# Kernel tuning notes

Measured on AMD Instinct MI355X. Metric: run time of the kernel, lower is better.

Reference implementation:

```python
import jax, jax.numpy as jnp
import numpy as np

N_NODES = 50000
N_EDGES = 800000
NUM_GRAPHS = 256
H = 128          # h_dim
C = H + 1        # CGConv channels = 129
Z = 2 * C + 1    # concat(x_i, x_j, edge_attr) = 259
N_GRAPH_LAYERS = 5
N_FC = 3
OUT_DIM = 1


def setup_inputs() -> dict:
    key = jax.random.key(0)
    ks = jax.random.split(key, 12)
    atoms = jax.random.randint(ks[0], (N_NODES,), 0, 119)
    pos = jax.random.normal(ks[1], (N_NODES, 3), dtype=jnp.float32)
    edge_index = jax.random.randint(ks[2], (2, N_EDGES), 0, N_NODES)
    batch = jnp.sort(jax.random.randint(ks[3], (N_NODES,), 0, NUM_GRAPHS))
    s = 0.05
    emb = jax.random.normal(ks[4], (119, H), dtype=jnp.float32)
    Wf = jax.random.normal(ks[5], (N_GRAPH_LAYERS, Z, C), dtype=jnp.float32) * s
    bf = jnp.zeros((N_GRAPH_LAYERS, C), dtype=jnp.float32)
    Ws = jax.random.normal(ks[6], (N_GRAPH_LAYERS, Z, C), dtype=jnp.float32) * s
    bs = jnp.zeros((N_GRAPH_LAYERS, C), dtype=jnp.float32)
    Wfc = jax.random.normal(ks[7], (N_FC, C, C), dtype=jnp.float32) * s
    bfc = jnp.zeros((N_FC, C), dtype=jnp.float32)
    Wout = jax.random.normal(ks[8], (C, OUT_DIM), dtype=jnp.float32) * s
    bout = jnp.zeros((OUT_DIM,), dtype=jnp.float32)
    return {"atoms": atoms, "pos": pos, "edge_index": edge_index, "batch": batch,
            "emb": emb, "Wf": Wf, "bf": bf, "Ws": Ws, "bs": bs,
            "Wfc": Wfc, "bfc": bfc, "Wout": Wout, "bout": bout}


def reference(atoms, pos, edge_index, batch, emb, Wf, bf, Ws, bs, Wfc, bfc, Wout, bout):
    n = atoms.shape[0]
    src, dst = edge_index[0], edge_index[1]  # PyG: x_j = x[src], x_i = x[dst], aggregate at dst
    # edge_attr = ||pos[src] - pos[dst]||, shape [E, 1]
    edge_attr = jnp.linalg.norm(pos[src] - pos[dst], axis=-1, keepdims=True)
    # node features: atom embedding + z-coordinate -> [N, 129]
    x = jnp.concatenate([emb[atoms], pos[:, 2:3]], axis=-1)
    for l in range(Wf.shape[0]):
        z = jnp.concatenate([x[dst], x[src], edge_attr], axis=-1)  # [E, 259]
        m = jax.nn.sigmoid(z @ Wf[l] + bf[l]) * jax.nn.softplus(z @ Ws[l] + bs[l])
        x = x + jax.ops.segment_sum(m, dst, num_segments=n)  # CGConv: aggr='add' + residual
    # mean pooling per graph
    sums = jax.ops.segment_sum(x, batch, num_segments=NUM_GRAPHS)
    cnts = jax.ops.segment_sum(jnp.ones((n, 1), x.dtype), batch, num_segments=NUM_GRAPHS)
    g = sums / jnp.maximum(cnts, 1.0)
    for l in range(Wfc.shape[0]):
        g = g @ Wfc[l] + bfc[l]
    return g @ Wout + bout
```

## Files before the change

kernel.cpp:

```cpp
#include <hip/hip_runtime.h>
#include <math.h>

#define N_NODES 50000
#define N_EDGES 800000
#define NUM_GRAPHS 256
#define NPADROWS 50048
#define CAP 64
#define SCLN -1.44269504088896f
#define SCLP 1.44269504088896f
#define C693 0.69314718056f
#define LROW 264

typedef __attribute__((ext_vector_type(8))) short short8;
typedef __attribute__((ext_vector_type(4))) float f32x4;
typedef __attribute__((ext_vector_type(2))) float f32x2;

__device__ __forceinline__ float fast_rcp(float x) {
#if __has_builtin(__builtin_amdgcn_rcpf)
  return __builtin_amdgcn_rcpf(x);
#else
  return 1.0f / x;
#endif
}
__device__ __forceinline__ float EX2(float x) {
#if __has_builtin(__builtin_amdgcn_exp2f)
  return __builtin_amdgcn_exp2f(x);
#else
  return exp2f(x);
#endif
}
__device__ __forceinline__ float LG2(float x) {
#if __has_builtin(__builtin_amdgcn_logf)
  return __builtin_amdgcn_logf(x);
#else
  return log2f(x);
#endif
}
__device__ __forceinline__ unsigned f2bf(float x) {
  unsigned u = __float_as_uint(x);
  return (u + 0x7fffu + ((u >> 16) & 1u)) >> 16;
}
__device__ __forceinline__ unsigned short bfr(float v) {
  return (unsigned short)((__float_as_uint(v) + 0x8000u) >> 16);
}
__device__ __forceinline__ unsigned pkbfr(float lo, float hi) {
  unsigned a = (__float_as_uint(lo) + 0x8000u) >> 16;
  unsigned b = (__float_as_uint(hi) + 0x8000u) & 0xffff0000u;
  return a | b;
}
__device__ __forceinline__ float u2f(unsigned u) { return __uint_as_float(u); }
__device__ __forceinline__ f32x2 mk2(float a, float b) {
  f32x2 r; r.x = a; r.y = b; return r;
}
__device__ __forceinline__ f32x2 unp(unsigned u) {
  return mk2(u2f(u << 16), u2f(u & 0xffff0000u));
}
__device__ __forceinline__ void edge_ch2(f32x2 gf, f32x2 gs, float cmul, f32x2& acc) {
  f32x2 den = mk2(EX2(gf.x), EX2(gf.y)) + 1.0f;
  f32x2 lg = mk2(LG2(1.0f + EX2(-fabsf(gs.x))), LG2(1.0f + EX2(-fabsf(gs.y))));
  f32x2 sp = lg + __builtin_elementwise_max(gs, (f32x2)0.0f);
  f32x2 rt = mk2(fast_rcp(den.x), fast_rcp(den.y)) * sp;
  acc = __builtin_elementwise_fma(rt, (f32x2)cmul, acc);
}

__global__ void init_x(const int* __restrict__ atoms, const float* __restrict__ pos,
                       const float* __restrict__ emb, float* __restrict__ x128c,
                       unsigned* __restrict__ xbu, float4* __restrict__ pos4,
                       int* __restrict__ cnt) {
  int n = blockIdx.x;
  int t = threadIdx.x;
  int a = atoms[n];
  float2 e = *(const float2*)(emb + (size_t)a * 128 + 2 * t);
  xbu[(size_t)n * 64 + t] = f2bf(e.x) | (f2bf(e.y) << 16);
  if (t == 0) x128c[n] = pos[n * 3 + 2];
  if (t == 1) pos4[n] = make_float4(pos[3 * n], pos[3 * n + 1], pos[3 * n + 2], 0.f);
  if (t == 2) cnt[n] = 0;
}

__global__ void prep_b(const float* __restrict__ Wf, const float* __restrict__ Ws,
                       const float* __restrict__ bfp, const float* __restrict__ bsp,
                       uint4* __restrict__ Bp, float2* __restrict__ Wtail) {
  int idx = blockIdx.x * 256 + threadIdx.x;
  if (idx < 5 * 4 * 9 * 4 * 64) {
    int lane = idx & 63;
    int t = idx >> 6;
    int ks = t & 3; t >>= 2;
    int ct = t % 9; t /= 9;
    int g = t & 3;
    int l = t >> 2;
    const float* W = (g >= 2) ? Ws : Wf;
    float sc = (g < 2) ? SCLN : SCLP;
    int col = ct * 16 + (lane & 15);
    int kb = ks * 32 + (lane >> 4) * 8;
    unsigned u[4];
#pragma unroll
    for (int p = 0; p < 4; ++p) {
      unsigned lo = 0, hi = 0;
      if (col < 129) {
        int k0 = kb + 2 * p, k1 = k0 + 1;
        int r0 = (g & 1) ? 129 + k0 : k0;
        int r1 = (g & 1) ? 129 + k1 : k1;
        lo = f2bf(sc * W[(size_t)(l * 259 + r0) * 129 + col]);
        hi = f2bf(sc * W[(size_t)(l * 259 + r1) * 129 + col]);
      }
      u[p] = lo | (hi << 16);
    }
    Bp[idx] = make_uint4(u[0], u[1], u[2], u[3]);
  } else {
    int j = idx - 5 * 4 * 9 * 4 * 64;
    if (j >= 5 * 4 * 144) return;
    int c = j % 144;
    int t = j / 144;
    int g = t & 3;
    int l = t >> 2;
    float sc = (g < 2) ? SCLN : SCLP;
    float w1 = 0.0f, bias = 0.0f;
    if (c <= 128) {
      const float* W = (g >= 2) ? Ws : Wf;
      int row = (g & 1) ? 257 : 128;
      w1 = sc * W[(size_t)(l * 259 + row) * 129 + c];
      if (g == 0) bias = SCLN * bfp[l * 129 + c];
      if (g == 2) bias = SCLP * bsp[l * 129 + c];
    }
    Wtail[(l * 4 + g) * 144 + c] = make_float2(w1, bias);
  }
}

__global__ void build_csr(const int* __restrict__ ei, const float4* __restrict__ pos4,
                          const int* __restrict__ batch, int* __restrict__ cnt,
                          int2* __restrict__ csr, int* __restrict__ goff) {
  int e = blockIdx.x * 256 + threadIdx.x;
  if (e <= N_NODES) {
    int b = (e < N_NODES) ? batch[e] : NUM_GRAPHS;
    int bp = (e > 0) ? batch[e - 1] : -1;
    for (int g = bp + 1; g <= b; ++g) goff[g] = e;
  }
  if (e >= N_EDGES) return;
  int s = ei[e];
  int d = ei[N_EDGES + e];
  float4 ps = pos4[s];
  float4 pd = pos4[d];
  float dx = ps.x - pd.x, dy = ps.y - pd.y, dz = ps.z - pd.z;
  float ea = sqrtf(dx * dx + dy * dy + dz * dz);
  int p = atomicAdd(&cnt[d], 1);
  if (p < CAP) csr[d * CAP + p] = make_int2(s, __float_as_int(ea));
}

__global__ __launch_bounds__(256) void gemm_mfma(
    const unsigned* __restrict__ xbu, const float* __restrict__ x128c,
    const uint4* __restrict__ Bp, const float2* __restrict__ Wtail,
    unsigned short* __restrict__ Pdh, unsigned short* __restrict__ Pfs,
    unsigned* __restrict__ Pd128c, unsigned* __restrict__ Pc128, int layer) {
  __shared__ short smA[32 * 136];
  __shared__ unsigned short ldsD[32 * LROW];
  __shared__ unsigned short ldsS[32 * LROW];
  int n0 = blockIdx.x * 32;
  int tid = threadIdx.x;
  for (int ch = tid; ch < 512; ch += 256) {
    int row = ch >> 4, cq = ch & 15;
    *(uint4*)(&smA[row * 136 + cq * 8]) =
        *(const uint4*)(xbu + (size_t)(n0 + row) * 64 + cq * 4);
  }
  __syncthreads();
  int g = tid >> 6;
  int l = tid & 63;
  int q = l >> 4, c16 = l & 15;
  const short8* Bp8 = (const short8*)Bp;
  int bbase = (layer * 4 + g) * 9 * 4;
  f32x4 acc[2][9];
#pragma unroll
  for (int rt = 0; rt < 2; ++rt)
#pragma unroll
    for (int ct = 0; ct < 9; ++ct) acc[rt][ct] = (f32x4){0.f, 0.f, 0.f, 0.f};
#pragma unroll
  for (int ks = 0; ks < 4; ++ks) {
    short8 a0 = *(const short8*)(&smA[c16 * 136 + (ks * 4 + q) * 8]);
    short8 a1 = *(const short8*)(&smA[(16 + c16) * 136 + (ks * 4 + q) * 8]);
#pragma unroll
    for (int ct = 0; ct < 9; ++ct) {
      short8 b = Bp8[(size_t)(bbase + ct * 4 + ks) * 64 + l];
      acc[0][ct] = __builtin_amdgcn_mfma_f32_16x16x32_bf16(a0, b, acc[0][ct], 0, 0, 0);
      acc[1][ct] = __builtin_amdgcn_mfma_f32_16x16x32_bf16(a1, b, acc[1][ct], 0, 0, 0);
    }
  }
  const float2* Wt = Wtail + (layer * 4 + g) * 144;
  float x128[2][4];
#pragma unroll
  for (int rt = 0; rt < 2; ++rt)
#pragma unroll
    for (int r = 0; r < 4; ++r)
      x128[rt][r] = x128c[n0 + rt * 16 + q * 4 + r];
  unsigned short* ldsO = (g & 1) ? ldsS : ldsD;
  int soff = (g >= 2) ? 2 : 0;
  unsigned short* c128p = (g & 1) ? (unsigned short*)Pc128 : (unsigned short*)Pd128c;
  int c128o = (g >= 2) ? 1 : 0;
#pragma unroll
  for (int ct = 0; ct < 9; ++ct) {
    int col = ct * 16 + c16;
    float2 wb = Wt[col];
#pragma unroll
    for (int rt = 0; rt < 2; ++rt) {
#pragma unroll
      for (int r = 0; r < 4; ++r) {
        int rl = rt * 16 + q * 4 + r;
        float v = acc[rt][ct][r] + fmaf(x128[rt][r], wb.x, wb.y);
        if (col < 128) {
          ldsO[rl * LROW + ((col >> 1) << 2) + soff + (col & 1)] = bfr(v);
        } else if (col == 128) {
          c128p[2 * (size_t)(n0 + rl) + c128o] = bfr(v);
        }
      }
    }
  }
  __syncthreads();
#pragma unroll
  for (int i = tid; i < 2048; i += 256) {
    int img = i >> 10;
    int c = i & 1023;
    int row = c >> 5, part = c & 31;
    const unsigned short* src = (img ? ldsS : ldsD) + row * LROW + part * 8;
    unsigned short* dst = (img ? Pfs : Pdh) + (size_t)(n0 + row) * 256 + part * 8;
    *(uint4*)dst = *(const uint4*)src;
  }
}

__global__ __launch_bounds__(256) void edge_agg(
    const unsigned short* __restrict__ Pdh, const unsigned short* __restrict__ Pfs,
    const unsigned* __restrict__ Pd128c, const unsigned* __restrict__ Pc128,
    unsigned* __restrict__ xbu, float* __restrict__ x128c, const int* __restrict__ cnt,
    const int2* __restrict__ csr, const float* __restrict__ WfL,
    const float* __restrict__ WsL) {
  int lane = threadIdx.x & 63;
  int half = lane >> 5;
  int l5 = lane & 31;
  int n = blockIdx.x * 4 + (threadIdx.x >> 6);
  if (n >= N_NODES) return;
  int nu = __builtin_amdgcn_readfirstlane(n);
  const float* wfl = WfL + 258 * 129;
  const float* wsl = WsL + 258 * 129;
  uint4 pdv = *(const uint4*)(Pdh + (size_t)nu * 256 + 8 * l5);
  f32x2 bfa = unp(pdv.x), bsa = unp(pdv.y), bfb = unp(pdv.z), bsb = unp(pdv.w);
  float2 wfa0 = *(const float2*)(wfl + 4 * l5);
  float2 wfb0 = *(const float2*)(wfl + 4 * l5 + 2);
  float2 wsa0 = *(const float2*)(wsl + 4 * l5);
  float2 wsb0 = *(const float2*)(wsl + 4 * l5 + 2);
  f32x2 wfa = mk2(SCLN * wfa0.x, SCLN * wfa0.y), wfb = mk2(SCLN * wfb0.x, SCLN * wfb0.y);
  f32x2 wsa = mk2(SCLP * wsa0.x, SCLP * wsa0.y), wsb = mk2(SCLP * wsb0.x, SCLP * wsb0.y);
  unsigned pd1 = Pd128c[nu];
  float bfc8 = u2f(pd1 << 16), bsc8 = u2f(pd1 & 0xffff0000u);
  float wfc8 = SCLN * wfl[128], wsc8 = SCLP * wsl[128];
  int m = cnt[nu];
  if (m > CAP) m = CAP;
  const int4* cb4 = (const int4*)(csr + (size_t)nu * CAP);
  const uint4* Pfq = (const uint4*)Pfs;
  float maskC = half ? 0.0f : C693;
  f32x2 accA = (f32x2)0.0f, accB = (f32x2)0.0f;

#define GATHER(qq) Pfq[(size_t)(half ? qq.z : qq.x) * 32 + l5]
#define COMPUTE(qq, gg, CM)                                                    \
  {                                                                            \
    f32x2 ea_ = (f32x2)__int_as_float(half ? qq.w : qq.y);                     \
    edge_ch2(__builtin_elementwise_fma(ea_, wfa, bfa + unp(gg.x)),             \
             __builtin_elementwise_fma(ea_, wsa, bsa + unp(gg.y)), CM, accA);  \
    edge_ch2(__builtin_elementwise_fma(ea_, wfb, bfb + unp(gg.z)),             \
             __builtin_elementwise_fma(ea_, wsb, bsb + unp(gg.w)), CM, accB);  \
  }

  int Pf = m >> 1;
  int4 qc = make_int4(0, 0, 0, 0);
  uint4 gc = make_uint4(0, 0, 0, 0);
  if (Pf > 0) {
    qc = cb4[0];
    gc = GATHER(qc);
  }
  for (int p = 0; p < Pf; ++p) {
    int4 qn = qc;
    uint4 gn = gc;
    if (p + 1 < Pf) {
      qn = cb4[p + 1];
      gn = GATHER(qn);
    }
    COMPUTE(qc, gc, C693);
    qc = qn;
    gc = gn;
  }
  if (m & 1) {
    int4 qt = cb4[Pf];
    f32x2 ea_ = (f32x2)__int_as_float(qt.y);
    uint4 gt = Pfq[(size_t)qt.x * 32 + l5];
    edge_ch2(__builtin_elementwise_fma(ea_, wfa, bfa + unp(gt.x)),
             __builtin_elementwise_fma(ea_, wsa, bsa + unp(gt.y)), maskC, accA);
    edge_ch2(__builtin_elementwise_fma(ea_, wfb, bfb + unp(gt.z)),
             __builtin_elementwise_fma(ea_, wsb, bsb + unp(gt.w)), maskC, accB);
  }
#undef GATHER
#undef COMPUTE

  accA.x += __shfl_xor(accA.x, 32, 64);
  accA.y += __shfl_xor(accA.y, 32, 64);
  accB.x += __shfl_xor(accB.x, 32, 64);
  accB.y += __shfl_xor(accB.y, 32, 64);

  float v2 = 0.f;
  if (lane < m) {
    int2 se = csr[(size_t)nu * CAP + lane];
    float ea = __int_as_float(se.y);
    unsigned pc = Pc128[se.x];
    float f2 = u2f(pc << 16), s2 = u2f(pc & 0xffff0000u);
    float gf2 = fmaf(ea, wfc8, bfc8 + f2);
    float gs2 = fmaf(ea, wsc8, bsc8 + s2);
    float sp2 = LG2(1.0f + EX2(-fabsf(gs2))) + fmaxf(gs2, 0.0f);
    v2 = C693 * fast_rcp(1.0f + EX2(gf2)) * sp2;
  }
#pragma unroll
  for (int off = 32; off; off >>= 1) v2 += __shfl_down(v2, off, 64);

  if (half == 0) {
    uint2 xv = *(const uint2*)(xbu + (size_t)nu * 64 + 2 * l5);
    f32x2 xa = unp(xv.x) + accA;
    f32x2 xb = unp(xv.y) + accB;
    *(uint2*)(xbu + (size_t)nu * 64 + 2 * l5) =
        make_uint2(pkbfr(xa.x, xa.y), pkbfr(xb.x, xb.y));
  }
  if (lane == 0) x128c[nu] += v2;
}

__global__ void pool2(const unsigned* __restrict__ xbu, const float* __restrict__ x128c,
                      const int* __restrict__ goff, float* __restrict__ gpart) {
  int gph = blockIdx.x >> 2;
  int q = blockIdx.x & 3;
  int t = threadIdx.x;
  if (t >= 129) return;
  int s = goff[gph], e = goff[gph + 1];
  int len = e - s;
  int chunk = (len + 3) >> 2;
  int a = s + q * chunk;
  int b = a + chunk; if (b > e) b = e;
  float acc = 0.f;
  if (t < 128) {
    int w = t >> 1, hi = t & 1;
    for (int n = a; n < b; ++n) {
      unsigned u = xbu[(size_t)n * 64 + w];
      acc += hi ? u2f(u & 0xffff0000u) : u2f(u << 16);
    }
  } else {
    for (int n = a; n < b; ++n) acc += x128c[n];
  }
  gpart[(size_t)(gph * 4 + q) * 132 + t] = acc;
}

__global__ void fcout(const float* __restrict__ gpart, const int* __restrict__ goff,
                      const float* __restrict__ Wfc, const float* __restrict__ bfc,
                      const float* __restrict__ Wout, const float* __restrict__ bout,
                      float* __restrict__ out) {
  __shared__ float buf[2][132];
  __shared__ float red[3];
  int i = blockIdx.x;
  int t = threadIdx.x;
  int len = goff[i + 1] - goff[i];
  float inv = fast_rcp(fmaxf((float)len, 1.0f));
  if (t < 129) {
    float v = gpart[(size_t)(i * 4 + 0) * 132 + t] + gpart[(size_t)(i * 4 + 1) * 132 + t] +
              gpart[(size_t)(i * 4 + 2) * 132 + t] + gpart[(size_t)(i * 4 + 3) * 132 + t];
    buf[0][t] = v * inv;
  }
  __syncthreads();
  int cur = 0;
#pragma unroll
  for (int l = 0; l < 3; ++l) {
    float s = 0.f;
    if (t < 129) {
      s = bfc[l * 129 + t];
      const float* W = Wfc + (size_t)l * 129 * 129;
#pragma unroll 4
      for (int k = 0; k < 129; ++k) s += buf[cur][k] * W[k * 129 + t];
    }
    __syncthreads();
    if (t < 129) buf[1 - cur][t] = s;
    cur = 1 - cur;
    __syncthreads();
  }
  float p = (t < 129) ? buf[cur][t] * Wout[t] : 0.f;
#pragma unroll
  for (int off = 32; off; off >>= 1) p += __shfl_down(p, off, 64);
  if ((t & 63) == 0) red[t >> 6] = p;
  __syncthreads();
  if (t == 0) out[i] = red[0] + red[1] + red[2] + bout[0];
}

extern "C" void kernel_launch(void* const* d_in, const int* in_sizes, int n_in,
                              void* d_out, int out_size, void* d_ws, size_t ws_size,
                              hipStream_t stream) {
  const int* atoms = (const int*)d_in[0];
  const float* pos = (const float*)d_in[1];
  const int* ei = (const int*)d_in[2];
  const int* batch = (const int*)d_in[3];
  const float* emb = (const float*)d_in[4];
  const float* Wf = (const float*)d_in[5];
  const float* bfp = (const float*)d_in[6];
  const float* Ws = (const float*)d_in[7];
  const float* bsp = (const float*)d_in[8];
  const float* Wfc = (const float*)d_in[9];
  const float* bfc = (const float*)d_in[10];
  const float* Wout = (const float*)d_in[11];
  const float* bout = (const float*)d_in[12];
  float* outp = (float*)d_out;

  uint4* Bp = (uint4*)d_ws;
  unsigned* xbu = (unsigned*)(Bp + 46080);
  unsigned short* Pdh = (unsigned short*)(xbu + (size_t)NPADROWS * 64);
  unsigned short* Pfs = Pdh + (size_t)NPADROWS * 256;
  float4* pos4 = (float4*)(Pfs + (size_t)NPADROWS * 256);
  float2* Wtail = (float2*)(pos4 + N_NODES);
  float* x128c = (float*)(Wtail + 5 * 4 * 144);
  float* gpart = x128c + NPADROWS;
  int* goff = (int*)(gpart + 256 * 4 * 132);
  int* cnt = goff + 260;
  int2* csr = (int2*)(cnt + N_NODES + 4);
  unsigned* Pd128c = (unsigned*)(csr + (size_t)N_NODES * CAP);
  unsigned* Pc128 = Pd128c + NPADROWS;

  init_x<<<N_NODES, 64, 0, stream>>>(atoms, pos, emb, x128c, xbu, pos4, cnt);
  prep_b<<<(5 * 4 * 9 * 4 * 64 + 5 * 4 * 144 + 255) / 256, 256, 0, stream>>>(
      Wf, Ws, bfp, bsp, Bp, Wtail);
  build_csr<<<(N_EDGES + 255) / 256, 256, 0, stream>>>(ei, pos4, batch, cnt, csr, goff);

  for (int l = 0; l < 5; ++l) {
    gemm_mfma<<<NPADROWS / 32, 256, 0, stream>>>(xbu, x128c, Bp, Wtail, Pdh, Pfs,
                                                 Pd128c, Pc128, l);
    edge_agg<<<(N_NODES + 3) / 4, 256, 0, stream>>>(Pdh, Pfs, Pd128c, Pc128, xbu, x128c,
                                                    cnt, csr,
                                                    Wf + (size_t)l * 259 * 129,
                                                    Ws + (size_t)l * 259 * 129);
  }

  pool2<<<NUM_GRAPHS * 4, 192, 0, stream>>>(xbu, x128c, goff, gpart);
  fcout<<<NUM_GRAPHS, 192, 0, stream>>>(gpart, goff, Wfc, bfc, Wout, bout, outp);
}
```

Measured before the change: 681.2 us.

## Permute GEMM output columns so MFMA results store directly to global

Weight packing now permutes columns so each lane's 8 MFMA column tiles map to 8 contiguous output channels. The GEMM epilogue then writes packed uint4 rows straight to global memory, with the f and s halves stored separately. This removes the LDS staging buffers, a barrier and the copy-out loop. The edge aggregation kernel changes its gathers from one uint4 to two uint2 loads (f half and s half) per source node, which adds load instructions in the hot edge loop.

```diff
diff --git a/kernel.cpp b/kernel.cpp
--- a/kernel.cpp
+++ b/kernel.cpp
@@ -9,7 +9,6 @@
 #define SCLN -1.44269504088896f
 #define SCLP 1.44269504088896f
 #define C693 0.69314718056f
-#define LROW 264
 
 typedef __attribute__((ext_vector_type(8))) short short8;
 typedef __attribute__((ext_vector_type(4))) float f32x4;
@@ -90,7 +89,8 @@
     int l = t >> 2;
     const float* W = (g >= 2) ? Ws : Wf;
     float sc = (g < 2) ? SCLN : SCLP;
-    int col = ct * 16 + (lane & 15);
+    int c16 = lane & 15;
+    int col = (ct < 8) ? (c16 * 8 + ct) : (c16 == 0 ? 128 : 999);
     int kb = ks * 32 + (lane >> 4) * 8;
     unsigned u[4];
 #pragma unroll
@@ -152,8 +152,6 @@
     unsigned short* __restrict__ Pdh, unsigned short* __restrict__ Pfs,
     unsigned* __restrict__ Pd128c, unsigned* __restrict__ Pc128, int layer) {
   __shared__ short smA[32 * 136];
-  __shared__ unsigned short ldsD[32 * LROW];
-  __shared__ unsigned short ldsS[32 * LROW];
   int n0 = blockIdx.x * 32;
   int tid = threadIdx.x;
   for (int ch = tid; ch < 512; ch += 256) {
@@ -184,43 +182,41 @@
     }
   }
   const float2* Wt = Wtail + (layer * 4 + g) * 144;
+  float2 wb[8];
+#pragma unroll
+  for (int ct = 0; ct < 8; ++ct) wb[ct] = Wt[c16 * 8 + ct];
+  float2 wb8 = Wt[128];
   float x128[2][4];
 #pragma unroll
   for (int rt = 0; rt < 2; ++rt)
 #pragma unroll
     for (int r = 0; r < 4; ++r)
       x128[rt][r] = x128c[n0 + rt * 16 + q * 4 + r];
-  unsigned short* ldsO = (g & 1) ? ldsS : ldsD;
-  int soff = (g >= 2) ? 2 : 0;
+  unsigned short* Pout = (g & 1) ? Pfs : Pdh;
+  int shalf = (g >= 2) ? 128 : 0;
   unsigned short* c128p = (g & 1) ? (unsigned short*)Pc128 : (unsigned short*)Pd128c;
   int c128o = (g >= 2) ? 1 : 0;
 #pragma unroll
-  for (int ct = 0; ct < 9; ++ct) {
-    int col = ct * 16 + c16;
-    float2 wb = Wt[col];
-#pragma unroll
-    for (int rt = 0; rt < 2; ++rt) {
-#pragma unroll
-      for (int r = 0; r < 4; ++r) {
-        int rl = rt * 16 + q * 4 + r;
-        float v = acc[rt][ct][r] + fmaf(x128[rt][r], wb.x, wb.y);
-        if (col < 128) {
-          ldsO[rl * LROW + ((col >> 1) << 2) + soff + (col & 1)] = bfr(v);
-        } else if (col == 128) {
-          c128p[2 * (size_t)(n0 + rl) + c128o] = bfr(v);
-        }
+  for (int rt = 0; rt < 2; ++rt) {
+#pragma unroll
+    for (int r = 0; r < 4; ++r) {
+      int node = n0 + rt * 16 + q * 4 + r;
+      float xv = x128[rt][r];
+      float v[8];
+#pragma unroll
+      for (int ct = 0; ct < 8; ++ct)
+        v[ct] = acc[rt][ct][r] + fmaf(xv, wb[ct].x, wb[ct].y);
+      uint4 pk;
+      pk.x = pkbfr(v[0], v[1]);
+      pk.y = pkbfr(v[2], v[3]);
+      pk.z = pkbfr(v[4], v[5]);
+      pk.w = pkbfr(v[6], v[7]);
+      *(uint4*)(Pout + (size_t)node * 256 + shalf + c16 * 8) = pk;
+      if (c16 == 0) {
+        float v8 = acc[rt][8][r] + fmaf(xv, wb8.x, wb8.y);
+        c128p[2 * (size_t)node + c128o] = bfr(v8);
       }
     }
-  }
-  __syncthreads();
-#pragma unroll
-  for (int i = tid; i < 2048; i += 256) {
-    int img = i >> 10;
-    int c = i & 1023;
-    int row = c >> 5, part = c & 31;
-    const unsigned short* src = (img ? ldsS : ldsD) + row * LROW + part * 8;
-    unsigned short* dst = (img ? Pfs : Pdh) + (size_t)(n0 + row) * 256 + part * 8;
-    *(uint4*)dst = *(const uint4*)src;
   }
 }
 
@@ -238,8 +234,9 @@
   int nu = __builtin_amdgcn_readfirstlane(n);
   const float* wfl = WfL + 258 * 129;
   const float* wsl = WsL + 258 * 129;
-  uint4 pdv = *(const uint4*)(Pdh + (size_t)nu * 256 + 8 * l5);
-  f32x2 bfa = unp(pdv.x), bsa = unp(pdv.y), bfb = unp(pdv.z), bsb = unp(pdv.w);
+  uint2 pdf = *(const uint2*)(Pdh + (size_t)nu * 256 + 4 * l5);
+  uint2 pds = *(const uint2*)(Pdh + (size_t)nu * 256 + 128 + 4 * l5);
+  f32x2 bfa = unp(pdf.x), bfb = unp(pdf.y), bsa = unp(pds.x), bsb = unp(pds.y);
   float2 wfa0 = *(const float2*)(wfl + 4 * l5);
   float2 wfb0 = *(const float2*)(wfl + 4 * l5 + 2);
   float2 wsa0 = *(const float2*)(wsl + 4 * l5);
@@ -252,48 +249,55 @@
   int m = cnt[nu];
   if (m > CAP) m = CAP;
   const int4* cb4 = (const int4*)(csr + (size_t)nu * CAP);
-  const uint4* Pfq = (const uint4*)Pfs;
+  const uint2* Pfq = (const uint2*)Pfs;
   float maskC = half ? 0.0f : C693;
   f32x2 accA = (f32x2)0.0f, accB = (f32x2)0.0f;
 
-#define GATHER(qq) Pfq[(size_t)(half ? qq.z : qq.x) * 32 + l5]
-#define COMPUTE(qq, gg, CM)                                                    \
+#define SRCOF(qq) ((size_t)(half ? qq.z : qq.x) * 64)
+#define COMPUTE(qq, uf, us, CM)                                                \
   {                                                                            \
     f32x2 ea_ = (f32x2)__int_as_float(half ? qq.w : qq.y);                     \
-    edge_ch2(__builtin_elementwise_fma(ea_, wfa, bfa + unp(gg.x)),             \
-             __builtin_elementwise_fma(ea_, wsa, bsa + unp(gg.y)), CM, accA);  \
-    edge_ch2(__builtin_elementwise_fma(ea_, wfb, bfb + unp(gg.z)),             \
-             __builtin_elementwise_fma(ea_, wsb, bsb + unp(gg.w)), CM, accB);  \
+    edge_ch2(__builtin_elementwise_fma(ea_, wfa, bfa + unp(uf.x)),             \
+             __builtin_elementwise_fma(ea_, wsa, bsa + unp(us.x)), CM, accA);  \
+    edge_ch2(__builtin_elementwise_fma(ea_, wfb, bfb + unp(uf.y)),             \
+             __builtin_elementwise_fma(ea_, wsb, bsb + unp(us.y)), CM, accB);  \
   }
 
   int Pf = m >> 1;
   int4 qc = make_int4(0, 0, 0, 0);
-  uint4 gc = make_uint4(0, 0, 0, 0);
+  uint2 fc = make_uint2(0, 0), sc = make_uint2(0, 0);
   if (Pf > 0) {
     qc = cb4[0];
-    gc = GATHER(qc);
+    size_t o = SRCOF(qc);
+    fc = Pfq[o + l5];
+    sc = Pfq[o + 32 + l5];
   }
   for (int p = 0; p < Pf; ++p) {
     int4 qn = qc;
-    uint4 gn = gc;
+    uint2 fn = fc, sn = sc;
     if (p + 1 < Pf) {
       qn = cb4[p + 1];
-      gn = GATHER(qn);
-    }
-    COMPUTE(qc, gc, C693);
+      size_t o = SRCOF(qn);
+      fn = Pfq[o + l5];
+      sn = Pfq[o + 32 + l5];
+    }
+    COMPUTE(qc, fc, sc, C693);
     qc = qn;
-    gc = gn;
+    fc = fn;
+    sc = sn;
   }
   if (m & 1) {
     int4 qt = cb4[Pf];
+    size_t o = (size_t)qt.x * 64;
+    uint2 ft = Pfq[o + l5];
+    uint2 st = Pfq[o + 32 + l5];
     f32x2 ea_ = (f32x2)__int_as_float(qt.y);
-    uint4 gt = Pfq[(size_t)qt.x * 32 + l5];
-    edge_ch2(__builtin_elementwise_fma(ea_, wfa, bfa + unp(gt.x)),
-             __builtin_elementwise_fma(ea_, wsa, bsa + unp(gt.y)), maskC, accA);
-    edge_ch2(__builtin_elementwise_fma(ea_, wfb, bfb + unp(gt.z)),
-             __builtin_elementwise_fma(ea_, wsb, bsb + unp(gt.w)), maskC, accB);
-  }
-#undef GATHER
+    edge_ch2(__builtin_elementwise_fma(ea_, wfa, bfa + unp(ft.x)),
+             __builtin_elementwise_fma(ea_, wsa, bsa + unp(st.x)), maskC, accA);
+    edge_ch2(__builtin_elementwise_fma(ea_, wfb, bfb + unp(ft.y)),
+             __builtin_elementwise_fma(ea_, wsb, bsb + unp(st.y)), maskC, accB);
+  }
+#undef SRCOF
 #undef COMPUTE
 
   accA.x += __shfl_xor(accA.x, 32, 64);
```

Result: no change. 681.7 us (+0.1%).
